# Performance work log

Hardware: AMD Instinct MI355X
Metric: run time of the kernel (lower is better)

The kernel has to match this reference:

```python
import jax, jax.numpy as jnp
import numpy as np

N_NODES = 100000
N_EDGES = 3200000
IN_DIM, HID_DIM, OUT_DIM = 384, 128, 5


def gcn_conv(x, src, dst, W, b, num_nodes):
    # PyG GCNConv: add self-loops, symmetric normalization, linear, aggregate, bias
    h = x @ W  # [N, out]
    ones = jnp.ones(src.shape[0], dtype=h.dtype)
    deg = jax.ops.segment_sum(ones, dst, num_segments=num_nodes)  # includes self-loops
    dinv = jnp.where(deg > 0, jax.lax.rsqrt(deg), 0.0)
    norm = dinv[src] * dinv[dst]  # [E+N]
    msg = h[src] * norm[:, None]
    out = jax.ops.segment_sum(msg, dst, num_segments=num_nodes)
    return out + b


def setup_inputs() -> dict:
    key = jax.random.key(0)
    ks = jax.random.split(key, 8)
    x = jax.random.normal(ks[0], (N_NODES, IN_DIM), dtype=jnp.float32)
    edge_index = jax.random.randint(ks[1], (2, N_EDGES), 0, N_NODES, dtype=jnp.int64)
    # Glorot-ish init for GCN linear weights
    def glorot(k, fi, fo):
        s = jnp.sqrt(6.0 / (fi + fo))
        return jax.random.uniform(k, (fi, fo), jnp.float32, -s, s)
    W1 = glorot(ks[2], IN_DIM, HID_DIM)
    b1 = jnp.zeros((HID_DIM,), jnp.float32)
    W2 = glorot(ks[3], HID_DIM, HID_DIM)
    b2 = jnp.zeros((HID_DIM,), jnp.float32)
    W3 = glorot(ks[4], HID_DIM, OUT_DIM)
    b3 = jnp.zeros((OUT_DIM,), jnp.float32)
    return {"x": x, "edge_index": edge_index, "W1": W1, "b1": b1,
            "W2": W2, "b2": b2, "W3": W3, "b3": b3}


def reference(x, edge_index, W1, b1, W2, b2, W3, b3):
    num_nodes = x.shape[0]
    loops = jnp.arange(num_nodes, dtype=edge_index.dtype)
    src = jnp.concatenate([edge_index[0], loops])
    dst = jnp.concatenate([edge_index[1], loops])
    # layer 1: GCNConv + ReLU (dropout is identity at inference)
    h = jax.nn.relu(gcn_conv(x, src, dst, W1, b1, num_nodes))
    # layer 2
    h = jax.nn.relu(gcn_conv(h, src, dst, W2, b2, num_nodes))
    # final layer: logits, no activation
    return gcn_conv(h, src, dst, W3, b3, num_nodes)
```

## Files before the change

### kernel.cpp

```cpp
#include <hip/hip_runtime.h>
#include <hip/hip_fp16.h>

#define NN 100000
#define NE 3200000
#define SCAN_CHUNK 1024

#define BSH 8
#define BKT_NODES 256
#define NBKT ((NN + BKT_NODES - 1) / BKT_NODES)
#define BIN_BLOCKS 256
#define EPB ((NE + BIN_BLOCKS - 1) / BIN_BLOCKS)
#define GH (NBKT * BIN_BLOCKS)

typedef unsigned int uint;
typedef unsigned short ushort;
typedef __attribute__((ext_vector_type(8))) _Float16 half8;
typedef __attribute__((ext_vector_type(4))) float f32x4;

__device__ inline void gload16(const void* g, void* l) {
    __builtin_amdgcn_global_load_lds(
        (const __attribute__((address_space(1))) void*)g,
        (__attribute__((address_space(3))) void*)l, 16, 0, 0);
}

__device__ inline uint f2h_pair(float a, float b) {
    return (uint)__half_as_ushort(__float2half(a)) |
           ((uint)__half_as_ushort(__float2half(b)) << 16);
}
__device__ inline float h2f_lo(uint u) { return __half2float(__ushort_as_half((ushort)(u & 0xFFFFu))); }
__device__ inline float h2f_hi(uint u) { return __half2float(__ushort_as_half((ushort)(u >> 16))); }
__device__ inline void splitH(float x, ushort& h, ushort& l) {
    __half hh = __float2half(x);
    h = __half_as_ushort(hh);
    l = __half_as_ushort(__float2half(x - __half2float(hh)));
}

__global__ __launch_bounds__(256) void hist_bkt(const int* __restrict__ dst,
                                                int* __restrict__ ghist) {
    __shared__ int h[NBKT];
    int t = threadIdx.x;
    for (int i = t; i < NBKT; i += 256) h[i] = 0;
    __syncthreads();
    int beg = blockIdx.x * EPB;
    int end = beg + EPB; if (end > NE) end = NE;
    for (int e = beg + t; e < end; e += 256)
        atomicAdd(&h[dst[e] >> BSH], 1);
    __syncthreads();
    for (int i = t; i < NBKT; i += 256)
        ghist[i * BIN_BLOCKS + blockIdx.x] = h[i];
}

__global__ __launch_bounds__(256) void scan_p1(const int* __restrict__ cnt,
                                               int* __restrict__ bsum, int N) {
    int t = threadIdx.x;
    int base = blockIdx.x * SCAN_CHUNK + t * 4;
    int s = 0;
#pragma unroll
    for (int q = 0; q < 4; q++) {
        int i = base + q;
        if (i < N) s += cnt[i];
    }
    __shared__ int red[4];
#pragma unroll
    for (int off = 32; off; off >>= 1) s += __shfl_down(s, off, 64);
    if ((t & 63) == 0) red[t >> 6] = s;
    __syncthreads();
    if (t == 0) bsum[blockIdx.x] = red[0] + red[1] + red[2] + red[3];
}

__global__ void scan_p2(int* __restrict__ bsum, int nb) {
    __shared__ int s[128];
    int t = threadIdx.x;
    int v = (t < nb) ? bsum[t] : 0;
    s[t] = v;
    __syncthreads();
    for (int off = 1; off < 128; off <<= 1) {
        int x = s[t];
        int add = (t >= off) ? s[t - off] : 0;
        __syncthreads();
        s[t] = x + add;
        __syncthreads();
    }
    if (t < nb) bsum[t] = s[t] - v;
}

__global__ __launch_bounds__(256) void scan_p3_plain(int* __restrict__ data,
                                                     const int* __restrict__ bsum, int N) {
    __shared__ int ts[256];
    int t = threadIdx.x;
    int base = blockIdx.x * SCAN_CHUNK + t * 4;
    int c[4];
    int s = 0;
#pragma unroll
    for (int q = 0; q < 4; q++) {
        int i = base + q;
        c[q] = (i < N) ? data[i] : 0;
        s += c[q];
    }
    ts[t] = s;
    __syncthreads();
    for (int off = 1; off < 256; off <<= 1) {
        int x = ts[t];
        int add = (t >= off) ? ts[t - off] : 0;
        __syncthreads();
        ts[t] = x + add;
        __syncthreads();
    }
    int run = bsum[blockIdx.x] + ts[t] - s;
#pragma unroll
    for (int q = 0; q < 4; q++) {
        int i = base + q;
        if (i < N) { data[i] = run; run += c[q]; }
    }
}

__global__ __launch_bounds__(256) void scan_p3_deg(const int* __restrict__ cnt,
                                                   const int* __restrict__ bsum,
                                                   int* __restrict__ rowptr,
                                                   float* __restrict__ dinv, int N) {
    __shared__ int ts[256];
    int t = threadIdx.x;
    int base = blockIdx.x * SCAN_CHUNK + t * 4;
    int c[4];
    int s = 0;
#pragma unroll
    for (int q = 0; q < 4; q++) {
        int i = base + q;
        c[q] = (i < N) ? cnt[i] : 0;
        s += c[q];
    }
    ts[t] = s;
    __syncthreads();
    for (int off = 1; off < 256; off <<= 1) {
        int x = ts[t];
        int add = (t >= off) ? ts[t - off] : 0;
        __syncthreads();
        ts[t] = x + add;
        __syncthreads();
    }
    int run = bsum[blockIdx.x] + ts[t] - s;
#pragma unroll
    for (int q = 0; q < 4; q++) {
        int i = base + q;
        if (i < N) {
            rowptr[i] = run;
            dinv[i] = 1.0f / sqrtf((float)(c[q] + 1));
            run += c[q];
        }
    }
    if (base < N && N <= base + 4) rowptr[N] = run;
}

__global__ __launch_bounds__(256) void bin_edges(const int* __restrict__ src,
                                                 const int* __restrict__ dst,
                                                 const int* __restrict__ ghist,
                                                 uint* __restrict__ binned) {
    __shared__ int cur[NBKT];
    int t = threadIdx.x;
    for (int i = t; i < NBKT; i += 256) cur[i] = ghist[i * BIN_BLOCKS + blockIdx.x];
    __syncthreads();
    int beg = blockIdx.x * EPB;
    int end = beg + EPB; if (end > NE) end = NE;
    for (int e = beg + t; e < end; e += 256) {
        int d = dst[e];
        int b = d >> BSH;
        int p = atomicAdd(&cur[b], 1);
        binned[p] = ((uint)src[e] << BSH) | (uint)(d & (BKT_NODES - 1));
    }
}

__global__ __launch_bounds__(256) void bucket_count(const uint* __restrict__ binned,
                                                    const int* __restrict__ ghist,
                                                    int* __restrict__ cnt) {
    __shared__ int c[BKT_NODES];
    int t = threadIdx.x;
    int bkt = blockIdx.x;
    for (int i = t; i < BKT_NODES; i += 256) c[i] = 0;
    __syncthreads();
    int beg = ghist[bkt * BIN_BLOCKS];
    int end = (bkt == NBKT - 1) ? NE : ghist[(bkt + 1) * BIN_BLOCKS];
    for (int j = beg + t; j < end; j += 256)
        atomicAdd(&c[binned[j] & (BKT_NODES - 1)], 1);
    __syncthreads();
    int base = bkt * BKT_NODES;
    int nb = NN - base; if (nb > BKT_NODES) nb = BKT_NODES;
    for (int i = t; i < nb; i += 256) cnt[base + i] = c[i];
}

__global__ __launch_bounds__(256) void csr_fill(const uint* __restrict__ binned,
                                                const int* __restrict__ ghist,
                                                const int* __restrict__ rowptr,
                                                int* __restrict__ col) {
    __shared__ int fill[BKT_NODES];
    int t = threadIdx.x;
    int bkt = blockIdx.x;
    for (int i = t; i < BKT_NODES; i += 256) fill[i] = 0;
    __syncthreads();
    int beg = ghist[bkt * BIN_BLOCKS];
    int end = (bkt == NBKT - 1) ? NE : ghist[(bkt + 1) * BIN_BLOCKS];
    int base = bkt * BKT_NODES;
    for (int j = beg + t; j < end; j += 256) {
        uint r = binned[j];
        int dl = r & (BKT_NODES - 1);
        int p = rowptr[base + dl] + atomicAdd(&fill[dl], 1);
        col[p] = (int)(r >> BSH);
    }
}

template <int K>
__global__ __launch_bounds__(256) void wsplit(const float* __restrict__ W,
                                              ushort* __restrict__ Wth,
                                              ushort* __restrict__ Wtl) {
    __shared__ float tile[32][128];
    int t = threadIdx.x;
    int kb = blockIdx.x;
    {
        int k = t >> 3, cq = t & 7;
#pragma unroll
        for (int q = 0; q < 4; q++) {
            float4 v = *(const float4*)&W[(size_t)(kb * 32 + k) * 128 + cq * 16 + q * 4];
            *(float4*)&tile[k][cq * 16 + q * 4] = v;
        }
    }
    __syncthreads();
    {
        int c = t >> 1, g = t & 1;
        ushort hs[16], ls[16];
#pragma unroll
        for (int i = 0; i < 16; i++) splitH(tile[g * 16 + i][c], hs[i], ls[i]);
        uint h[8], lo[8];
#pragma unroll
        for (int i = 0; i < 8; i++) {
            h[i] = (uint)hs[2 * i] | ((uint)hs[2 * i + 1] << 16);
            lo[i] = (uint)ls[2 * i] | ((uint)ls[2 * i + 1] << 16);
        }
        size_t o = (size_t)c * K + kb * 32 + g * 16;
        *(uint4*)&Wth[o] = make_uint4(h[0], h[1], h[2], h[3]);
        *(uint4*)&Wth[o + 8] = make_uint4(h[4], h[5], h[6], h[7]);
        *(uint4*)&Wtl[o] = make_uint4(lo[0], lo[1], lo[2], lo[3]);
        *(uint4*)&Wtl[o + 8] = make_uint4(lo[4], lo[5], lo[6], lo[7]);
    }
}

template <int K>
__global__ __launch_bounds__(256) void mfma_gemm_f32(const float* __restrict__ X,
                                                     const ushort* __restrict__ Wth,
                                                     const ushort* __restrict__ Wtl,
                                                     const float* __restrict__ dinv,
                                                     uint* __restrict__ Y, int M) {
    __shared__ char smem[24 * 1024];
    char* aP = smem;
    char* bH = smem + 8192;
    char* bL = smem + 16384;
    int tid = threadIdx.x;
    int w = tid >> 6, l = tid & 63;
    int rowBase = blockIdx.x * 128;

    f32x4 acc[2][8];
#pragma unroll
    for (int mf = 0; mf < 2; mf++)
#pragma unroll
        for (int n = 0; n < 8; n++) acc[mf][n] = (f32x4){0.f, 0.f, 0.f, 0.f};

    int sRow = tid >> 1, sKp = tid & 1;
    int gRow = rowBase + sRow;
    bool rowOK = gRow < M;
    size_t aBase = (size_t)(rowOK ? gRow : 0) * K + sKp * 16;

    float4 a0, a1, a2, a3;
    a0 = a1 = a2 = a3 = make_float4(0.f, 0.f, 0.f, 0.f);
    if (rowOK) {
        a0 = *(const float4*)&X[aBase];
        a1 = *(const float4*)&X[aBase + 4];
        a2 = *(const float4*)&X[aBase + 8];
        a3 = *(const float4*)&X[aBase + 12];
    }

    int fc = l & 15, fkg = l >> 4;
    int aoff0 = fkg * 2048 + ((2 * w + 0) * 16 + fc) * 16;
    int aoff1 = fkg * 2048 + ((2 * w + 1) * 16 + fc) * 16;

    for (int kt = 0; kt < K; kt += 32) {
#pragma unroll
        for (int i = 0; i < 2; i++) {
            int cb = (i * 4 + w) * 64;
            int c = cb + l;
            int kg = c >> 7, colb = c & 127;
            size_t go = (size_t)colb * K + kt + kg * 8;
            gload16(&Wth[go], bH + cb * 16);
            gload16(&Wtl[go], bL + cb * 16);
        }
        {
            float v[16] = {a0.x, a0.y, a0.z, a0.w, a1.x, a1.y, a1.z, a1.w,
                           a2.x, a2.y, a2.z, a2.w, a3.x, a3.y, a3.z, a3.w};
            uint hh[8];
#pragma unroll
            for (int i = 0; i < 8; i++) hh[i] = f2h_pair(v[2 * i], v[2 * i + 1]);
            *(uint4*)(aP + (2 * sKp) * 2048 + sRow * 16) = make_uint4(hh[0], hh[1], hh[2], hh[3]);
            *(uint4*)(aP + (2 * sKp + 1) * 2048 + sRow * 16) = make_uint4(hh[4], hh[5], hh[6], hh[7]);
        }
        __syncthreads();

        if (kt + 32 < K && rowOK) {
            size_t nb = aBase + kt + 32;
            a0 = *(const float4*)&X[nb];
            a1 = *(const float4*)&X[nb + 4];
            a2 = *(const float4*)&X[nb + 8];
            a3 = *(const float4*)&X[nb + 12];
        }

        half8 av0 = *(const half8*)(aP + aoff0);
        half8 av1 = *(const half8*)(aP + aoff1);
#pragma unroll
        for (int n = 0; n < 8; n++) {
            int boff = fkg * 2048 + (16 * n + fc) * 16;
            half8 bh = *(const half8*)(bH + boff);
            half8 bl = *(const half8*)(bL + boff);
            acc[0][n] = __builtin_amdgcn_mfma_f32_16x16x32_f16(av0, bh, acc[0][n], 0, 0, 0);
            acc[0][n] = __builtin_amdgcn_mfma_f32_16x16x32_f16(av0, bl, acc[0][n], 0, 0, 0);
            acc[1][n] = __builtin_amdgcn_mfma_f32_16x16x32_f16(av1, bh, acc[1][n], 0, 0, 0);
            acc[1][n] = __builtin_amdgcn_mfma_f32_16x16x32_f16(av1, bl, acc[1][n], 0, 0, 0);
        }
        __syncthreads();
    }

#pragma unroll
    for (int mf = 0; mf < 2; mf++) {
        float dscale[4];
#pragma unroll
        for (int r = 0; r < 4; r++) {
            int row = rowBase + (2 * w + mf) * 16 + fkg * 4 + r;
            dscale[r] = (row < M) ? dinv[row] : 0.f;
        }
#pragma unroll
        for (int n = 0; n < 8; n++) {
#pragma unroll
            for (int r = 0; r < 4; r++) {
                float val = acc[mf][n][r] * dscale[r];
                float p = __shfl_xor(val, 1, 64);
                int row = rowBase + (2 * w + mf) * 16 + fkg * 4 + r;
                if (!(l & 1) && row < M)
                    Y[(size_t)row * 64 + 8 * n + (fc >> 1)] = f2h_pair(val, p);
            }
        }
    }
}

__global__ __launch_bounds__(256) void mfma_gemm_f16(const ushort* __restrict__ Xh,
                                                     const ushort* __restrict__ Wth,
                                                     const ushort* __restrict__ Wtl,
                                                     const float* __restrict__ dinv,
                                                     uint* __restrict__ Y, int M) {
    __shared__ char smem[24 * 1024];
    char* aP = smem;
    char* bH = smem + 8192;
    char* bL = smem + 16384;
    int tid = threadIdx.x;
    int w = tid >> 6, l = tid & 63;
    int rowBase = blockIdx.x * 128;

    f32x4 acc[2][8];
#pragma unroll
    for (int mf = 0; mf < 2; mf++)
#pragma unroll
        for (int n = 0; n < 8; n++) acc[mf][n] = (f32x4){0.f, 0.f, 0.f, 0.f};

    int fc = l & 15, fkg = l >> 4;
    int aoff0 = fkg * 2048 + ((2 * w + 0) * 16 + fc) * 16;
    int aoff1 = fkg * 2048 + ((2 * w + 1) * 16 + fc) * 16;

    for (int kt = 0; kt < 128; kt += 32) {
#pragma unroll
        for (int i = 0; i < 2; i++) {
            int cb = (i * 4 + w) * 64;
            int c = cb + l;
            int kg = c >> 7, idx = c & 127;
            gload16(&Xh[(size_t)(rowBase + idx) * 128 + kt + kg * 8], aP + cb * 16);
            gload16(&Wth[(size_t)idx * 128 + kt + kg * 8], bH + cb * 16);
            gload16(&Wtl[(size_t)idx * 128 + kt + kg * 8], bL + cb * 16);
        }
        __syncthreads();
        half8 av0 = *(const half8*)(aP + aoff0);
        half8 av1 = *(const half8*)(aP + aoff1);
#pragma unroll
        for (int n = 0; n < 8; n++) {
            int boff = fkg * 2048 + (16 * n + fc) * 16;
            half8 bh = *(const half8*)(bH + boff);
            half8 bl = *(const half8*)(bL + boff);
            acc[0][n] = __builtin_amdgcn_mfma_f32_16x16x32_f16(av0, bh, acc[0][n], 0, 0, 0);
            acc[0][n] = __builtin_amdgcn_mfma_f32_16x16x32_f16(av0, bl, acc[0][n], 0, 0, 0);
            acc[1][n] = __builtin_amdgcn_mfma_f32_16x16x32_f16(av1, bh, acc[1][n], 0, 0, 0);
            acc[1][n] = __builtin_amdgcn_mfma_f32_16x16x32_f16(av1, bl, acc[1][n], 0, 0, 0);
        }
        __syncthreads();
    }

#pragma unroll
    for (int mf = 0; mf < 2; mf++) {
        float dscale[4];
#pragma unroll
        for (int r = 0; r < 4; r++) {
            int row = rowBase + (2 * w + mf) * 16 + fkg * 4 + r;
            dscale[r] = (row < M) ? dinv[row] : 0.f;
        }
#pragma unroll
        for (int n = 0; n < 8; n++) {
#pragma unroll
            for (int r = 0; r < 4; r++) {
                float val = acc[mf][n][r] * dscale[r];
                float p = __shfl_xor(val, 1, 64);
                int row = rowBase + (2 * w + mf) * 16 + fkg * 4 + r;
                if (!(l & 1) && row < M)
                    Y[(size_t)row * 64 + 8 * n + (fc >> 1)] = f2h_pair(val, p);
            }
        }
    }
}

__global__ __launch_bounds__(256) void gemm_n5h(const uint4* __restrict__ Xh,
                                                const float* __restrict__ W,
                                                float* __restrict__ Y, int M) {
    __shared__ float wl[640];
    int t = threadIdx.x;
    for (int i = t; i < 640; i += 256) wl[i] = W[i];
    __syncthreads();
    int row = blockIdx.x * 256 + t;
    if (row >= M) return;
    float acc0 = 0.f, acc1 = 0.f, acc2 = 0.f, acc3 = 0.f, acc4 = 0.f;
#pragma unroll
    for (int kq = 0; kq < 16; kq++) {
        uint4 v = Xh[(size_t)row * 16 + kq];
        uint uu[4] = {v.x, v.y, v.z, v.w};
#pragma unroll
        for (int e = 0; e < 4; e++) {
            float x0 = h2f_lo(uu[e]);
            float x1 = h2f_hi(uu[e]);
            int k = kq * 8 + e * 2;
            acc0 = fmaf(x0, wl[k * 5 + 0], acc0); acc0 = fmaf(x1, wl[k * 5 + 5], acc0);
            acc1 = fmaf(x0, wl[k * 5 + 1], acc1); acc1 = fmaf(x1, wl[k * 5 + 6], acc1);
            acc2 = fmaf(x0, wl[k * 5 + 2], acc2); acc2 = fmaf(x1, wl[k * 5 + 7], acc2);
            acc3 = fmaf(x0, wl[k * 5 + 3], acc3); acc3 = fmaf(x1, wl[k * 5 + 8], acc3);
            acc4 = fmaf(x0, wl[k * 5 + 4], acc4); acc4 = fmaf(x1, wl[k * 5 + 9], acc4);
        }
    }
    Y[row * 5 + 0] = acc0;
    Y[row * 5 + 1] = acc1;
    Y[row * 5 + 2] = acc2;
    Y[row * 5 + 3] = acc3;
    Y[row * 5 + 4] = acc4;
}

__global__ void pack5(const float* __restrict__ Y, const float* __restrict__ dinv,
                      uint4* __restrict__ hc, int N) {
    int node = blockIdx.x * 256 + threadIdx.x;
    if (node >= N) return;
    float di = dinv[node];
    float v0 = Y[node * 5 + 0] * di;
    float v1 = Y[node * 5 + 1] * di;
    float v2 = Y[node * 5 + 2] * di;
    float v3 = Y[node * 5 + 3] * di;
    float v4 = Y[node * 5 + 4] * di;
    hc[node] = make_uint4(f2h_pair(v0, v1), f2h_pair(v2, v3), f2h_pair(v4, 0.f), 0u);
}

#define ACC8H(v)                              \
    a0 += h2f_lo(v.x); a1 += h2f_hi(v.x);     \
    a2 += h2f_lo(v.y); a3 += h2f_hi(v.y);     \
    a4 += h2f_lo(v.z); a5 += h2f_hi(v.z);     \
    a6 += h2f_lo(v.w); a7 += h2f_hi(v.w);

__global__ __launch_bounds__(256) void agg128_v3(const uint4* __restrict__ hb4,
                                                 const int* __restrict__ rowptr,
                                                 const int* __restrict__ col,
                                                 const float* __restrict__ dinv,
                                                 const float* __restrict__ bias,
                                                 uint4* __restrict__ out, int N, int do_relu) {
    int wave = threadIdx.x >> 6;
    int lane = threadIdx.x & 63;
    int node = blockIdx.x * 4 + wave;
    if (node >= N) return;
    int g = lane >> 4;
    int q = lane & 15;
    int beg = rowptr[node], end = rowptr[node + 1];
    float a0 = 0.f, a1 = 0.f, a2 = 0.f, a3 = 0.f, a4 = 0.f, a5 = 0.f, a6 = 0.f, a7 = 0.f;

    int j = beg;
    for (; j + 16 <= end; j += 16) {
        int s0 = col[j + g];
        int s1 = col[j + 4 + g];
        int s2 = col[j + 8 + g];
        int s3 = col[j + 12 + g];
        uint4 v0 = hb4[(size_t)s0 * 16 + q];
        uint4 v1 = hb4[(size_t)s1 * 16 + q];
        uint4 v2 = hb4[(size_t)s2 * 16 + q];
        uint4 v3 = hb4[(size_t)s3 * 16 + q];
        ACC8H(v0); ACC8H(v1); ACC8H(v2); ACC8H(v3);
    }
    if (j + 8 <= end) {
        int s0 = col[j + g];
        int s1 = col[j + 4 + g];
        uint4 v0 = hb4[(size_t)s0 * 16 + q];
        uint4 v1 = hb4[(size_t)s1 * 16 + q];
        ACC8H(v0); ACC8H(v1);
        j += 8;
    }
    if (j < end) {
        int jj0 = j + g, jj1 = j + 4 + g;
        bool p0 = jj0 < end, p1 = jj1 < end;
        int s0 = p0 ? col[jj0] : node;
        int s1 = p1 ? col[jj1] : node;
        uint4 v0 = hb4[(size_t)s0 * 16 + q];
        uint4 v1 = hb4[(size_t)s1 * 16 + q];
        if (!p0) v0 = make_uint4(0u, 0u, 0u, 0u);
        if (!p1) v1 = make_uint4(0u, 0u, 0u, 0u);
        ACC8H(v0); ACC8H(v1);
    }
#pragma unroll
    for (int off = 16; off <= 32; off <<= 1) {
        a0 += __shfl_xor(a0, off, 64);
        a1 += __shfl_xor(a1, off, 64);
        a2 += __shfl_xor(a2, off, 64);
        a3 += __shfl_xor(a3, off, 64);
        a4 += __shfl_xor(a4, off, 64);
        a5 += __shfl_xor(a5, off, 64);
        a6 += __shfl_xor(a6, off, 64);
        a7 += __shfl_xor(a7, off, 64);
    }
    if (g == 0) {
        uint4 vs = hb4[(size_t)node * 16 + q];
        ACC8H(vs);
        float di = dinv[node];
        const float4* bias4 = (const float4*)bias;
        float4 bb0 = bias4[q * 2], bb1 = bias4[q * 2 + 1];
        float o0 = a0 * di + bb0.x, o1 = a1 * di + bb0.y;
        float o2 = a2 * di + bb0.z, o3 = a3 * di + bb0.w;
        float o4 = a4 * di + bb1.x, o5 = a5 * di + bb1.y;
        float o6 = a6 * di + bb1.z, o7 = a7 * di + bb1.w;
        if (do_relu) {
            o0 = fmaxf(o0, 0.f); o1 = fmaxf(o1, 0.f);
            o2 = fmaxf(o2, 0.f); o3 = fmaxf(o3, 0.f);
            o4 = fmaxf(o4, 0.f); o5 = fmaxf(o5, 0.f);
            o6 = fmaxf(o6, 0.f); o7 = fmaxf(o7, 0.f);
        }
        out[(size_t)node * 16 + q] =
            make_uint4(f2h_pair(o0, o1), f2h_pair(o2, o3), f2h_pair(o4, o5), f2h_pair(o6, o7));
    }
}

__global__ void agg5_v2(const uint4* __restrict__ hc, const int* __restrict__ rowptr,
                        const int* __restrict__ col, const float* __restrict__ dinv,
                        const float* __restrict__ b3, float* __restrict__ out, int N) {
    int node = blockIdx.x * 256 + threadIdx.x;
    if (node >= N) return;
    float a0 = 0.f, a1 = 0.f, a2 = 0.f, a3 = 0.f, a4 = 0.f;
    int beg = rowptr[node], end = rowptr[node + 1];
#pragma unroll 2
    for (int j = beg; j < end; ++j) {
        uint4 v = hc[col[j]];
        a0 += h2f_lo(v.x); a1 += h2f_hi(v.x);
        a2 += h2f_lo(v.y); a3 += h2f_hi(v.y);
        a4 += h2f_lo(v.z);
    }
    uint4 vs = hc[node];
    a0 += h2f_lo(vs.x); a1 += h2f_hi(vs.x);
    a2 += h2f_lo(vs.y); a3 += h2f_hi(vs.y);
    a4 += h2f_lo(vs.z);
    float di = dinv[node];
    out[node * 5 + 0] = a0 * di + b3[0];
    out[node * 5 + 1] = a1 * di + b3[1];
    out[node * 5 + 2] = a2 * di + b3[2];
    out[node * 5 + 3] = a3 * di + b3[3];
    out[node * 5 + 4] = a4 * di + b3[4];
}

static inline size_t align512(size_t x) { return (x + 511) & ~(size_t)511; }

extern "C" void kernel_launch(void* const* d_in, const int* in_sizes, int n_in,
                              void* d_out, int out_size, void* d_ws, size_t ws_size,
                              hipStream_t stream) {
    const float* x  = (const float*)d_in[0];
    const int* ei   = (const int*)d_in[1];
    const float* W1 = (const float*)d_in[2];
    const float* b1 = (const float*)d_in[3];
    const float* W2 = (const float*)d_in[4];
    const float* b2 = (const float*)d_in[5];
    const float* W3 = (const float*)d_in[6];
    const float* b3 = (const float*)d_in[7];
    const int* src = ei;
    const int* dst = ei + NE;

    char* ws = (char*)d_ws;
    size_t off = 0;
    int* cnt = (int*)(ws + off);        off += align512((size_t)NN * 4);
    int* rowptr = (int*)(ws + off);     off += align512((size_t)(NN + 1) * 4);
    float* dinv = (float*)(ws + off);   off += align512((size_t)NN * 4);
    int* bsum = (int*)(ws + off);       off += align512((size_t)128 * 4);
    int* ghist = (int*)(ws + off);      off += align512((size_t)GH * 4);
    ushort* wt1h = (ushort*)(ws + off); off += align512((size_t)128 * 384 * 2);
    ushort* wt1l = (ushort*)(ws + off); off += align512((size_t)128 * 384 * 2);
    ushort* wt2h = (ushort*)(ws + off); off += align512((size_t)128 * 128 * 2);
    ushort* wt2l = (ushort*)(ws + off); off += align512((size_t)128 * 128 * 2);
    int* col = (int*)(ws + off);        off += align512((size_t)NE * 4);
    uint* hb = (uint*)(ws + off);       off += align512((size_t)NN * 64 * 4);
    char* bufF = (char*)(ws + off);     off += align512((size_t)NN * 128 * 4);
    float* bufC = (float*)(ws + off);   off += align512((size_t)NN * 5 * 4);
    uint4* hc = (uint4*)(ws + off);     off += align512((size_t)NN * 16);
    uint* binned = (uint*)bufF;
    (void)ws_size;

    wsplit<384><<<12, 256, 0, stream>>>(W1, wt1h, wt1l);
    wsplit<128><<<4, 256, 0, stream>>>(W2, wt2h, wt2l);

    hist_bkt<<<BIN_BLOCKS, 256, 0, stream>>>(dst, ghist);
    {
        int nb = (GH + SCAN_CHUNK - 1) / SCAN_CHUNK;
        scan_p1<<<nb, 256, 0, stream>>>(ghist, bsum, GH);
        scan_p2<<<1, 128, 0, stream>>>(bsum, nb);
        scan_p3_plain<<<nb, 256, 0, stream>>>(ghist, bsum, GH);
    }
    bin_edges<<<BIN_BLOCKS, 256, 0, stream>>>(src, dst, ghist, binned);
    bucket_count<<<NBKT, 256, 0, stream>>>(binned, ghist, cnt);
    {
        int nb = (NN + SCAN_CHUNK - 1) / SCAN_CHUNK;
        scan_p1<<<nb, 256, 0, stream>>>(cnt, bsum, NN);
        scan_p2<<<1, 128, 0, stream>>>(bsum, nb);
        scan_p3_deg<<<nb, 256, 0, stream>>>(cnt, bsum, rowptr, dinv, NN);
    }
    csr_fill<<<NBKT, 256, 0, stream>>>(binned, ghist, rowptr, col);

    int gemm_blocks = (NN + 127) / 128;
    mfma_gemm_f32<384><<<gemm_blocks, 256, 0, stream>>>(x, wt1h, wt1l, dinv, hb, NN);
    agg128_v3<<<(NN + 3) / 4, 256, 0, stream>>>((const uint4*)hb, rowptr, col, dinv, b1,
                                                (uint4*)bufF, NN, 1);
    mfma_gemm_f16<<<gemm_blocks, 256, 0, stream>>>((const ushort*)bufF, wt2h, wt2l, dinv, hb, NN);
    agg128_v3<<<(NN + 3) / 4, 256, 0, stream>>>((const uint4*)hb, rowptr, col, dinv, b2,
                                                (uint4*)bufF, NN, 1);
    gemm_n5h<<<(NN + 255) / 256, 256, 0, stream>>>((const uint4*)bufF, W3, bufC, NN);
    pack5<<<(NN + 255) / 256, 256, 0, stream>>>(bufC, dinv, hc, NN);
    agg5_v2<<<(NN + 255) / 256, 256, 0, stream>>>(hc, rowptr, col, dinv, b3, (float*)d_out, NN);
}
```

Measured before the change: 427.8 us.

## Sort binned edges by source within buckets and fuse final GEMM with pack

Adds a per-bucket LDS counting sort that reorders each bucket's binned edge records by their high source bits, so the CSR column lists come out roughly ordered by source. This should make the gathers in the aggregation kernels more local. It also folds the dinv scaling and fp16 packing of the 5-wide final layer into the GEMM kernel, which drops one launch and an intermediate buffer. The trade-off is an extra sort pass over all edges, and buckets larger than the LDS capacity are silently left unsorted.

```diff
diff --git a/kernel.cpp b/kernel.cpp
--- a/kernel.cpp
+++ b/kernel.cpp
@@ -11,6 +11,7 @@
 #define BIN_BLOCKS 256
 #define EPB ((NE + BIN_BLOCKS - 1) / BIN_BLOCKS)
 #define GH (NBKT * BIN_BLOCKS)
+#define SORT_CAP 9216
 
 typedef unsigned int uint;
 typedef unsigned short ushort;
@@ -166,6 +167,47 @@
         int b = d >> BSH;
         int p = atomicAdd(&cur[b], 1);
         binned[p] = ((uint)src[e] << BSH) | (uint)(d & (BKT_NODES - 1));
+    }
+}
+
+__global__ __launch_bounds__(256) void sort_bucket(uint* __restrict__ binned,
+                                                   const int* __restrict__ ghist) {
+    __shared__ uint rec[SORT_CAP];
+    __shared__ int hist[512];
+    __shared__ int ts[256];
+    int t = threadIdx.x;
+    int bkt = blockIdx.x;
+    int beg = ghist[bkt * BIN_BLOCKS];
+    int end = (bkt == NBKT - 1) ? NE : ghist[(bkt + 1) * BIN_BLOCKS];
+    int n = end - beg;
+    if (n > SORT_CAP) return;
+    for (int i = t; i < 512; i += 256) hist[i] = 0;
+    __syncthreads();
+    for (int i = t; i < n; i += 256) {
+        uint r = binned[beg + i];
+        rec[i] = r;
+        atomicAdd(&hist[r >> 16], 1);
+    }
+    __syncthreads();
+    int h0 = hist[2 * t], h1 = hist[2 * t + 1];
+    int s = h0 + h1;
+    ts[t] = s;
+    __syncthreads();
+    for (int off = 1; off < 256; off <<= 1) {
+        int x = ts[t];
+        int add = (t >= off) ? ts[t - off] : 0;
+        __syncthreads();
+        ts[t] = x + add;
+        __syncthreads();
+    }
+    int excl = ts[t] - s;
+    hist[2 * t] = excl;
+    hist[2 * t + 1] = excl + h0;
+    __syncthreads();
+    for (int i = t; i < n; i += 256) {
+        uint r = rec[i];
+        int p = atomicAdd(&hist[r >> 16], 1);
+        binned[beg + p] = r;
     }
 }
 
@@ -419,7 +461,8 @@
 
 __global__ __launch_bounds__(256) void gemm_n5h(const uint4* __restrict__ Xh,
                                                 const float* __restrict__ W,
-                                                float* __restrict__ Y, int M) {
+                                                const float* __restrict__ dinv,
+                                                uint4* __restrict__ hc, int M) {
     __shared__ float wl[640];
     int t = threadIdx.x;
     for (int i = t; i < 640; i += 256) wl[i] = W[i];
@@ -443,24 +486,10 @@
             acc4 = fmaf(x0, wl[k * 5 + 4], acc4); acc4 = fmaf(x1, wl[k * 5 + 9], acc4);
         }
     }
-    Y[row * 5 + 0] = acc0;
-    Y[row * 5 + 1] = acc1;
-    Y[row * 5 + 2] = acc2;
-    Y[row * 5 + 3] = acc3;
-    Y[row * 5 + 4] = acc4;
-}
-
-__global__ void pack5(const float* __restrict__ Y, const float* __restrict__ dinv,
-                      uint4* __restrict__ hc, int N) {
-    int node = blockIdx.x * 256 + threadIdx.x;
-    if (node >= N) return;
-    float di = dinv[node];
-    float v0 = Y[node * 5 + 0] * di;
-    float v1 = Y[node * 5 + 1] * di;
-    float v2 = Y[node * 5 + 2] * di;
-    float v3 = Y[node * 5 + 3] * di;
-    float v4 = Y[node * 5 + 4] * di;
-    hc[node] = make_uint4(f2h_pair(v0, v1), f2h_pair(v2, v3), f2h_pair(v4, 0.f), 0u);
+    float di = dinv[row];
+    hc[row] = make_uint4(f2h_pair(acc0 * di, acc1 * di),
+                         f2h_pair(acc2 * di, acc3 * di),
+                         f2h_pair(acc4 * di, 0.f), 0u);
 }
 
 #define ACC8H(v)                              \
@@ -603,7 +632,6 @@
     int* col = (int*)(ws + off);        off += align512((size_t)NE * 4);
     uint* hb = (uint*)(ws + off);       off += align512((size_t)NN * 64 * 4);
     char* bufF = (char*)(ws + off);     off += align512((size_t)NN * 128 * 4);
-    float* bufC = (float*)(ws + off);   off += align512((size_t)NN * 5 * 4);
     uint4* hc = (uint4*)(ws + off);     off += align512((size_t)NN * 16);
     uint* binned = (uint*)bufF;
     (void)ws_size;
@@ -619,6 +647,7 @@
         scan_p3_plain<<<nb, 256, 0, stream>>>(ghist, bsum, GH);
     }
     bin_edges<<<BIN_BLOCKS, 256, 0, stream>>>(src, dst, ghist, binned);
+    sort_bucket<<<NBKT, 256, 0, stream>>>(binned, ghist);
     bucket_count<<<NBKT, 256, 0, stream>>>(binned, ghist, cnt);
     {
         int nb = (NN + SCAN_CHUNK - 1) / SCAN_CHUNK;
@@ -635,7 +664,6 @@
     mfma_gemm_f16<<<gemm_blocks, 256, 0, stream>>>((const ushort*)bufF, wt2h, wt2l, dinv, hb, NN);
     agg128_v3<<<(NN + 3) / 4, 256, 0, stream>>>((const uint4*)hb, rowptr, col, dinv, b2,
                                                 (uint4*)bufF, NN, 1);
-    gemm_n5h<<<(NN + 255) / 256, 256, 0, stream>>>((const uint4*)bufF, W3, bufC, NN);
-    pack5<<<(NN + 255) / 256, 256, 0, stream>>>(bufC, dinv, hc, NN);
+    gemm_n5h<<<(NN + 255) / 256, 256, 0, stream>>>((const uint4*)bufF, W3, dinv, hc, NN);
     agg5_v2<<<(NN + 255) / 256, 256, 0, stream>>>(hc, rowptr, col, dinv, b3, (float*)d_out, NN);
 }
```

Result: slower. 446.3 us (+4.3%).
